# Performance work log

Hardware: AMD Instinct MI355X
Metric: run time of the kernel (lower is better)

Reference implementation:

```python
import jax, jax.numpy as jnp
import numpy as np

N_NODES = 10000
EPS = 1e-5


def _layernorm(x, gamma, beta):
    mu = jnp.mean(x, axis=-1, keepdims=True)
    var = jnp.mean(jnp.square(x - mu), axis=-1, keepdims=True)
    return (x - mu) * jax.lax.rsqrt(var + EPS) * gamma + beta


def _sage_pool_layer(h, src, dst, Wp, bp, Ws, Wn, b, gamma, beta):
    # DGL SAGEConv(aggregator='pool'):
    #   m_u = relu(h_u @ Wp^T + bp); h_neigh[v] = max_{u in N(v)} m_u (0 if no neighbors)
    #   rst = h @ Ws^T + h_neigh @ Wn^T + b
    m = jax.nn.relu(h @ Wp.T + bp)              # [N, d]
    msg = m[src]                                 # [E, d] gather
    agg = jax.ops.segment_max(msg, dst, num_segments=N_NODES)
    agg = jnp.where(jnp.isfinite(agg), agg, 0.0)  # isolated nodes -> 0
    rst = h @ Ws.T + agg @ Wn.T + b
    # gsage_layer: LayerNorm, then Encoder applies relu (dropout inactive in eval)
    return jax.nn.relu(_layernorm(rst, gamma, beta))


def setup_inputs() -> dict:
    key = jax.random.key(0)
    ks = jax.random.split(key, 16)
    d = 256
    E = 320000
    s = 1.0 / np.sqrt(d)
    inp = {
        "h": jax.random.normal(ks[0], (N_NODES, d), dtype=jnp.float32),
        "edge_src": jax.random.randint(ks[1], (E,), 0, N_NODES, dtype=jnp.int32),
        "edge_dst": jax.random.randint(ks[2], (E,), 0, N_NODES, dtype=jnp.int32),
    }
    for li in range(2):
        kk = jax.random.split(ks[3 + li], 3)
        inp[f"Wp{li}"] = jax.random.normal(kk[0], (d, d), dtype=jnp.float32) * s
        inp[f"bp{li}"] = jnp.zeros((d,), jnp.float32)
        inp[f"Ws{li}"] = jax.random.normal(kk[1], (d, d), dtype=jnp.float32) * s
        inp[f"Wn{li}"] = jax.random.normal(kk[2], (d, d), dtype=jnp.float32) * s
        inp[f"b{li}"] = jnp.zeros((d,), jnp.float32)
        inp[f"g{li}"] = jnp.ones((d,), jnp.float32)
        inp[f"be{li}"] = jnp.zeros((d,), jnp.float32)
    return inp


def reference(h, edge_src, edge_dst,
              Wp0, bp0, Ws0, Wn0, b0, g0, be0,
              Wp1, bp1, Ws1, Wn1, b1, g1, be1):
    h = _sage_pool_layer(h, edge_src, edge_dst, Wp0, bp0, Ws0, Wn0, b0, g0, be0)
    h = _sage_pool_layer(h, edge_src, edge_dst, Wp1, bp1, Ws1, Wn1, b1, g1, be1)
    return h
```

## Files before the change

kernel.cpp:

```cpp
#include <hip/hip_runtime.h>

#define D 256
#define CAP 128
#define ASTRIDE 280
#define LN_EPS 1e-5f

typedef short short8 __attribute__((ext_vector_type(8)));
typedef float floatx4 __attribute__((ext_vector_type(4)));
typedef unsigned short u16x4 __attribute__((ext_vector_type(4)));

typedef const __attribute__((address_space(1))) void* gas_t;
typedef __attribute__((address_space(3))) void* las_t;

#define WAIT_VM(n) __builtin_amdgcn_s_waitcnt(((n) & 0xF) | (((n) >> 4) << 14) | (7 << 4) | (0xF << 8))

__device__ __forceinline__ u16x4 umax4(u16x4 a, u16x4 b) {
#if __has_builtin(__builtin_elementwise_max)
    return __builtin_elementwise_max(a, b);
#else
    u16x4 r;
    r.x = a.x > b.x ? a.x : b.x; r.y = a.y > b.y ? a.y : b.y;
    r.z = a.z > b.z ? a.z : b.z; r.w = a.w > b.w ? a.w : b.w;
    return r;
#endif
}

__device__ __forceinline__ unsigned short f2b(float f) {
    union { float f; unsigned int u; } x; x.f = f;
    unsigned int u = x.u + 0x7FFFu + ((x.u >> 16) & 1u);
    return (unsigned short)(u >> 16);
}

__global__ __launch_bounds__(256) void prep_kernel(
    const float* __restrict__ w0, const float* __restrict__ w1,
    const float* __restrict__ w2, const float* __restrict__ w3,
    const float* __restrict__ w4, const float* __restrict__ w5,
    unsigned short* __restrict__ wb,
    const float* __restrict__ h, unsigned short* __restrict__ hb, int nh4,
    int* __restrict__ cnt, unsigned short* __restrict__ mb, int N)
{
    const int blk = blockIdx.x;
    const int tid = threadIdx.x;
    if (blk < 384) {
        const int wsel = blk >> 6;
        const float* src;
        switch (wsel) {
            case 0: src = w0; break; case 1: src = w1; break;
            case 2: src = w2; break; case 3: src = w3; break;
            case 4: src = w4; break; default: src = w5; break;
        }
        const int idx = (blk & 63) * 1024 + tid * 4;
        const float4 v = *(const float4*)(src + idx);
        ushort4 o;
        o.x = f2b(v.x); o.y = f2b(v.y); o.z = f2b(v.z); o.w = f2b(v.w);
        *(ushort4*)(wb + (size_t)wsel * 65536 + idx) = o;
    } else if (blk < 1024) {
        int i = (blk - 384) * 256 + tid;
        const int stride = 640 * 256;
        for (; i < nh4; i += stride) {
            const float4 v = *(const float4*)(h + (size_t)i * 4);
            ushort4 o;
            o.x = f2b(v.x); o.y = f2b(v.y); o.z = f2b(v.z); o.w = f2b(v.w);
            *(ushort4*)(hb + (size_t)i * 4) = o;
        }
    } else if (blk < 1064) {
        const int i = (blk - 1024) * 256 + tid;
        if (i < N) cnt[i] = 0;
    } else {
        mb[(size_t)N * D + tid] = 0;
    }
}

__global__ __launch_bounds__(256) void gemm_relu(
    const unsigned short* __restrict__ A, const unsigned short* __restrict__ W,
    const float* __restrict__ bias, unsigned short* __restrict__ out_b, int N,
    const int* __restrict__ esrc, const int* __restrict__ edst,
    int* __restrict__ cnt, unsigned short* __restrict__ csr, int E, int ngemm)
{
    if ((int)blockIdx.x >= ngemm) {
        const int nsb = gridDim.x - ngemm;
        int i = ((int)blockIdx.x - ngemm) * 256 + threadIdx.x;
        const int stride = nsb * 256;
        for (; i < E; i += stride) {
            const int d = edst[i];
            const int pos = atomicAdd(&cnt[d], 1);
            if (pos < CAP) csr[(size_t)d * CAP + pos] = (unsigned short)esrc[i];
        }
        return;
    }

    const int tid = threadIdx.x;
    const int wave = tid >> 6;
    const int lane = tid & 63;
    const int quad = lane >> 4;
    const int l16 = lane & 15;
    const int row0 = blockIdx.x * 16;
    const int koff = quad * 8;

    floatx4 acc[4];
#pragma unroll
    for (int t = 0; t < 4; t++) acc[t] = (floatx4)(0.f);

    const unsigned short* aptr = A + (size_t)(row0 + l16) * D + koff;
    const unsigned short* wptr = W + (size_t)(wave * 64 + l16) * D + koff;
#pragma unroll
    for (int k0 = 0; k0 < D; k0 += 32) {
        const short8 av = *(const short8*)(aptr + k0);
        const short8 b0 = *(const short8*)(wptr + k0);
        const short8 b1 = *(const short8*)(wptr + 16 * D + k0);
        const short8 b2 = *(const short8*)(wptr + 32 * D + k0);
        const short8 b3 = *(const short8*)(wptr + 48 * D + k0);
        acc[0] = __builtin_amdgcn_mfma_f32_16x16x32_bf16(av, b0, acc[0], 0, 0, 0);
        acc[1] = __builtin_amdgcn_mfma_f32_16x16x32_bf16(av, b1, acc[1], 0, 0, 0);
        acc[2] = __builtin_amdgcn_mfma_f32_16x16x32_bf16(av, b2, acc[2], 0, 0, 0);
        acc[3] = __builtin_amdgcn_mfma_f32_16x16x32_bf16(av, b3, acc[3], 0, 0, 0);
    }

#pragma unroll
    for (int t = 0; t < 4; t++) {
        const float bcol = bias[wave * 64 + t * 16 + l16];
#pragma unroll
        for (int r = 0; r < 4; r++) {
            const int rg = row0 + quad * 4 + r;
            const int col = wave * 64 + t * 16 + l16;
            out_b[(size_t)rg * D + col] = f2b(fmaxf(acc[t][r] + bcol, 0.f));
        }
    }
}

__global__ __launch_bounds__(256, 3) void gemm_ln_pool(
    const unsigned short* __restrict__ A, const unsigned short* __restrict__ Wself,
    const unsigned short* __restrict__ Wneigh,
    const unsigned short* __restrict__ mpool,
    const int* __restrict__ cnt, const unsigned short* __restrict__ csr,
    const float* __restrict__ bias,
    const float* __restrict__ gamma, const float* __restrict__ beta,
    unsigned short* __restrict__ out_b, float* __restrict__ out_f, int N)
{
    __shared__ unsigned short idxS[16][CAP];
    __shared__ unsigned short gbuf[4][2][8][D];
    __shared__ unsigned short aggS[16 * ASTRIDE];
    __shared__ float redS[4][16], redS2[4][16], muA[16], rsA[16];

    const int tid = threadIdx.x;
    const int wave = tid >> 6;
    const int lane = tid & 63;
    const int quad = lane >> 4;
    const int l16 = lane & 15;
    const int row0 = blockIdx.x * 16;
    const int koff = quad * 8;
    const int rbase = wave * 4;
    const int half = lane >> 5;
    const int l32 = lane & 31;

    int degs[4];
#pragma unroll
    for (int rr = 0; rr < 4; rr++) degs[rr] = min(cnt[row0 + rbase + rr], CAP);
    int P = max(max(degs[0], degs[1]), max(degs[2], degs[3]));
    const int P2 = (P + 1) & ~1;
#pragma unroll
    for (int rr = 0; rr < 4; rr++) {
        const int rg = row0 + rbase + rr;
        for (int i = lane; i < P2; i += 64)
            idxS[rbase + rr][i] = (i < degs[rr]) ? csr[(size_t)rg * CAP + i]
                                                 : (unsigned short)N;
    }

    floatx4 acc[4];
#pragma unroll
    for (int t = 0; t < 4; t++) acc[t] = (floatx4)(0.f);

    {
        const unsigned short* aptr = A + (size_t)(row0 + l16) * D + koff;
        const unsigned short* wptr = Wself + (size_t)(wave * 64 + l16) * D + koff;
#pragma unroll
        for (int k0 = 0; k0 < D; k0 += 32) {
            const short8 av = *(const short8*)(aptr + k0);
            const short8 b0 = *(const short8*)(wptr + k0);
            const short8 b1 = *(const short8*)(wptr + 16 * D + k0);
            const short8 b2 = *(const short8*)(wptr + 32 * D + k0);
            const short8 b3 = *(const short8*)(wptr + 48 * D + k0);
            acc[0] = __builtin_amdgcn_mfma_f32_16x16x32_bf16(av, b0, acc[0], 0, 0, 0);
            acc[1] = __builtin_amdgcn_mfma_f32_16x16x32_bf16(av, b1, acc[1], 0, 0, 0);
            acc[2] = __builtin_amdgcn_mfma_f32_16x16x32_bf16(av, b2, acc[2], 0, 0, 0);
            acc[3] = __builtin_amdgcn_mfma_f32_16x16x32_bf16(av, b3, acc[3], 0, 0, 0);
        }
    }

    {
        const int nb = P2 >> 1;
        u16x4 mx[4];
#pragma unroll
        for (int rr = 0; rr < 4; rr++) mx[rr] = (u16x4)(0);

#define ISSUE_BURST(bi, buf)                                                    \
        {                                                                       \
            _Pragma("unroll") for (int rr = 0; rr < 4; rr++) {                  \
                const int jj = idxS[rbase + rr][2 * (bi) + half];               \
                const unsigned short* g = mpool + (size_t)jj * D + l32 * 8;     \
                __builtin_amdgcn_global_load_lds(                               \
                    (gas_t)g, (las_t)&gbuf[wave][buf][rr * 2][0], 16, 0, 0);    \
            }                                                                   \
        }

        if (nb > 0) ISSUE_BURST(0, 0);
        if (nb > 1) ISSUE_BURST(1, 1);
        for (int b = 0; b < nb; b++) {
            if (b + 1 < nb) WAIT_VM(4); else WAIT_VM(0);
            const int buf = b & 1;
#pragma unroll
            for (int rr = 0; rr < 4; rr++) {
                const u16x4 a0 = *(const u16x4*)&gbuf[wave][buf][rr * 2 + 0][lane * 4];
                const u16x4 a1 = *(const u16x4*)&gbuf[wave][buf][rr * 2 + 1][lane * 4];
                mx[rr] = umax4(mx[rr], umax4(a0, a1));
            }
            if (b + 2 < nb) ISSUE_BURST(b + 2, buf);
        }
#undef ISSUE_BURST
#pragma unroll
        for (int rr = 0; rr < 4; rr++)
            *(u16x4*)&aggS[(rbase + rr) * ASTRIDE + lane * 4] = mx[rr];
    }
    __syncthreads();

    {
        const unsigned short* wptr = Wneigh + (size_t)(wave * 64 + l16) * D + koff;
#pragma unroll
        for (int k0 = 0; k0 < D; k0 += 32) {
            const short8 av = *(const short8*)&aggS[l16 * ASTRIDE + koff + k0];
            const short8 b0 = *(const short8*)(wptr + k0);
            const short8 b1 = *(const short8*)(wptr + 16 * D + k0);
            const short8 b2 = *(const short8*)(wptr + 32 * D + k0);
            const short8 b3 = *(const short8*)(wptr + 48 * D + k0);
            acc[0] = __builtin_amdgcn_mfma_f32_16x16x32_bf16(av, b0, acc[0], 0, 0, 0);
            acc[1] = __builtin_amdgcn_mfma_f32_16x16x32_bf16(av, b1, acc[1], 0, 0, 0);
            acc[2] = __builtin_amdgcn_mfma_f32_16x16x32_bf16(av, b2, acc[2], 0, 0, 0);
            acc[3] = __builtin_amdgcn_mfma_f32_16x16x32_bf16(av, b3, acc[3], 0, 0, 0);
        }
    }

    float bcol[4];
#pragma unroll
    for (int t = 0; t < 4; t++) bcol[t] = bias[wave * 64 + t * 16 + l16];
#pragma unroll
    for (int t = 0; t < 4; t++)
#pragma unroll
        for (int r = 0; r < 4; r++) acc[t][r] += bcol[t];

#pragma unroll
    for (int r = 0; r < 4; r++) {
        float s = 0.f, s2 = 0.f;
#pragma unroll
        for (int t = 0; t < 4; t++) {
            const float v = acc[t][r];
            s += v; s2 += v * v;
        }
        s += __shfl_xor(s, 1);  s2 += __shfl_xor(s2, 1);
        s += __shfl_xor(s, 2);  s2 += __shfl_xor(s2, 2);
        s += __shfl_xor(s, 4);  s2 += __shfl_xor(s2, 4);
        s += __shfl_xor(s, 8);  s2 += __shfl_xor(s2, 8);
        if (l16 == 0) {
            redS[wave][quad * 4 + r] = s;
            redS2[wave][quad * 4 + r] = s2;
        }
    }
    __syncthreads();
    if (tid < 16) {
        const float S  = redS[0][tid] + redS[1][tid] + redS[2][tid] + redS[3][tid];
        const float S2 = redS2[0][tid] + redS2[1][tid] + redS2[2][tid] + redS2[3][tid];
        const float mu = S * (1.f / D);
        float var = S2 * (1.f / D) - mu * mu;
        var = fmaxf(var, 0.f);
        muA[tid] = mu;
        rsA[tid] = rsqrtf(var + LN_EPS);
    }
    __syncthreads();

    float gcol[4], becol[4];
#pragma unroll
    for (int t = 0; t < 4; t++) {
        gcol[t] = gamma[wave * 64 + t * 16 + l16];
        becol[t] = beta[wave * 64 + t * 16 + l16];
    }
#pragma unroll
    for (int r = 0; r < 4; r++) {
        const int rl = quad * 4 + r;
        const int rg = row0 + rl;
        const float mu = muA[rl];
        const float rs = rsA[rl];
#pragma unroll
        for (int t = 0; t < 4; t++) {
            const int col = wave * 64 + t * 16 + l16;
            float o = (acc[t][r] - mu) * rs * gcol[t] + becol[t];
            o = fmaxf(o, 0.f);
            if (out_f) out_f[(size_t)rg * D + col] = o;
            else       out_b[(size_t)rg * D + col] = f2b(o);
        }
    }
}

extern "C" void kernel_launch(void* const* d_in, const int* in_sizes, int n_in,
                              void* d_out, int out_size, void* d_ws, size_t ws_size,
                              hipStream_t stream) {
    const float* h    = (const float*)d_in[0];
    const int*   esrc = (const int*)d_in[1];
    const int*   edst = (const int*)d_in[2];
    const float* Wp0  = (const float*)d_in[3];
    const float* bp0  = (const float*)d_in[4];
    const float* Ws0  = (const float*)d_in[5];
    const float* Wn0  = (const float*)d_in[6];
    const float* b0   = (const float*)d_in[7];
    const float* g0   = (const float*)d_in[8];
    const float* be0  = (const float*)d_in[9];
    const float* Wp1  = (const float*)d_in[10];
    const float* bp1  = (const float*)d_in[11];
    const float* Ws1  = (const float*)d_in[12];
    const float* Wn1  = (const float*)d_in[13];
    const float* b1   = (const float*)d_in[14];
    const float* g1   = (const float*)d_in[15];
    const float* be1  = (const float*)d_in[16];

    const int N = in_sizes[0] / D;
    const int E = in_sizes[1];
    const size_t ND = (size_t)N * D;

    unsigned short* hb  = (unsigned short*)d_ws;
    unsigned short* mb  = hb + ND;
    unsigned short* h1b = mb + ND + D;
    unsigned short* wb  = h1b + ND;
    int* cnt = (int*)(wb + 6 * 65536);
    unsigned short* csr = (unsigned short*)(cnt + N);

    unsigned short* wpb0 = wb + 0 * 65536;
    unsigned short* wsb0 = wb + 1 * 65536;
    unsigned short* wnb0 = wb + 2 * 65536;
    unsigned short* wpb1 = wb + 3 * 65536;
    unsigned short* wsb1 = wb + 4 * 65536;
    unsigned short* wnb1 = wb + 5 * 65536;

    const int gblocks = N / 16;
    const int sblocks = 128;

    prep_kernel<<<1065, 256, 0, stream>>>(Wp0, Ws0, Wn0, Wp1, Ws1, Wn1, wb,
                                          h, hb, (int)(ND / 4), cnt, mb, N);

    gemm_relu<<<gblocks + sblocks, 256, 0, stream>>>(hb, wpb0, bp0, mb, N,
                                                     esrc, edst, cnt, csr, E, gblocks);
    gemm_ln_pool<<<gblocks, 256, 0, stream>>>(hb, wsb0, wnb0, mb, cnt, csr,
                                              b0, g0, be0, h1b, nullptr, N);

    gemm_relu<<<gblocks, 256, 0, stream>>>(h1b, wpb1, bp1, mb, N,
                                           esrc, edst, cnt, csr, 0, gblocks);
    gemm_ln_pool<<<gblocks, 256, 0, stream>>>(h1b, wsb1, wnb1, mb, cnt, csr,
                                              b1, g1, be1, nullptr, (float*)d_out, N);
}
```

Measured before the change: 222.2 us.

## Batch GEMM fragment loads and deepen neighbor-gather bursts to four rows

Restructures the MFMA loops so that all A and B fragments for half of K are loaded up front, giving more loads in flight before the MFMAs run. Each neighbor max-pool burst now gathers four neighbor rows per target node instead of two, with a doubled LDS gather buffer and a higher vmcnt wait threshold. Launch-bound occupancy hints change, and more scatter blocks are used for CSR construction. The trade-off is higher register and LDS use, which lowers occupancy in the pool kernel, and extra padding work for low-degree nodes.

```diff
diff --git a/kernel.cpp b/kernel.cpp
--- a/kernel.cpp
+++ b/kernel.cpp
@@ -30,6 +30,22 @@
     unsigned int u = x.u + 0x7FFFu + ((x.u >> 16) & 1u);
     return (unsigned short)(u >> 16);
 }
+
+#define GEMM_HALF(APTR_EXPR, WPTR, K0H)                                         \
+    {                                                                           \
+        short8 aF[4], bF[4][4];                                                 \
+        _Pragma("unroll") for (int ks = 0; ks < 4; ks++)                        \
+            aF[ks] = APTR_EXPR(K0H + ks * 32);                                  \
+        _Pragma("unroll") for (int ks = 0; ks < 4; ks++)                        \
+        _Pragma("unroll") for (int t = 0; t < 4; t++)                           \
+            bF[ks][t] = *(const short8*)((WPTR) + t * 16 * D + (K0H) + ks * 32);\
+        _Pragma("unroll") for (int ks = 0; ks < 4; ks++) {                      \
+            acc[0] = __builtin_amdgcn_mfma_f32_16x16x32_bf16(aF[ks], bF[ks][0], acc[0], 0, 0, 0); \
+            acc[1] = __builtin_amdgcn_mfma_f32_16x16x32_bf16(aF[ks], bF[ks][1], acc[1], 0, 0, 0); \
+            acc[2] = __builtin_amdgcn_mfma_f32_16x16x32_bf16(aF[ks], bF[ks][2], acc[2], 0, 0, 0); \
+            acc[3] = __builtin_amdgcn_mfma_f32_16x16x32_bf16(aF[ks], bF[ks][3], acc[3], 0, 0, 0); \
+        }                                                                       \
+    }
 
 __global__ __launch_bounds__(256) void prep_kernel(
     const float* __restrict__ w0, const float* __restrict__ w1,
@@ -71,7 +87,7 @@
     }
 }
 
-__global__ __launch_bounds__(256) void gemm_relu(
+__global__ __launch_bounds__(256, 4) void gemm_relu(
     const unsigned short* __restrict__ A, const unsigned short* __restrict__ W,
     const float* __restrict__ bias, unsigned short* __restrict__ out_b, int N,
     const int* __restrict__ esrc, const int* __restrict__ edst,
@@ -103,18 +119,10 @@
 
     const unsigned short* aptr = A + (size_t)(row0 + l16) * D + koff;
     const unsigned short* wptr = W + (size_t)(wave * 64 + l16) * D + koff;
-#pragma unroll
-    for (int k0 = 0; k0 < D; k0 += 32) {
-        const short8 av = *(const short8*)(aptr + k0);
-        const short8 b0 = *(const short8*)(wptr + k0);
-        const short8 b1 = *(const short8*)(wptr + 16 * D + k0);
-        const short8 b2 = *(const short8*)(wptr + 32 * D + k0);
-        const short8 b3 = *(const short8*)(wptr + 48 * D + k0);
-        acc[0] = __builtin_amdgcn_mfma_f32_16x16x32_bf16(av, b0, acc[0], 0, 0, 0);
-        acc[1] = __builtin_amdgcn_mfma_f32_16x16x32_bf16(av, b1, acc[1], 0, 0, 0);
-        acc[2] = __builtin_amdgcn_mfma_f32_16x16x32_bf16(av, b2, acc[2], 0, 0, 0);
-        acc[3] = __builtin_amdgcn_mfma_f32_16x16x32_bf16(av, b3, acc[3], 0, 0, 0);
-    }
+#define A_GLOBAL(K) (*(const short8*)(aptr + (K)))
+    GEMM_HALF(A_GLOBAL, wptr, 0)
+    GEMM_HALF(A_GLOBAL, wptr, 128)
+#undef A_GLOBAL
 
 #pragma unroll
     for (int t = 0; t < 4; t++) {
@@ -128,7 +136,7 @@
     }
 }
 
-__global__ __launch_bounds__(256, 3) void gemm_ln_pool(
+__global__ __launch_bounds__(256, 2) void gemm_ln_pool(
     const unsigned short* __restrict__ A, const unsigned short* __restrict__ Wself,
     const unsigned short* __restrict__ Wneigh,
     const unsigned short* __restrict__ mpool,
@@ -138,7 +146,7 @@
     unsigned short* __restrict__ out_b, float* __restrict__ out_f, int N)
 {
     __shared__ unsigned short idxS[16][CAP];
-    __shared__ unsigned short gbuf[4][2][8][D];
+    __shared__ unsigned short gbuf[4][2][16][D];
     __shared__ unsigned short aggS[16 * ASTRIDE];
     __shared__ float redS[4][16], redS2[4][16], muA[16], rsA[16];
 
@@ -157,11 +165,11 @@
 #pragma unroll
     for (int rr = 0; rr < 4; rr++) degs[rr] = min(cnt[row0 + rbase + rr], CAP);
     int P = max(max(degs[0], degs[1]), max(degs[2], degs[3]));
-    const int P2 = (P + 1) & ~1;
+    const int P4 = (P + 3) & ~3;
 #pragma unroll
     for (int rr = 0; rr < 4; rr++) {
         const int rg = row0 + rbase + rr;
-        for (int i = lane; i < P2; i += 64)
+        for (int i = lane; i < P4; i += 64)
             idxS[rbase + rr][i] = (i < degs[rr]) ? csr[(size_t)rg * CAP + i]
                                                  : (unsigned short)N;
     }
@@ -173,22 +181,14 @@
     {
         const unsigned short* aptr = A + (size_t)(row0 + l16) * D + koff;
         const unsigned short* wptr = Wself + (size_t)(wave * 64 + l16) * D + koff;
-#pragma unroll
-        for (int k0 = 0; k0 < D; k0 += 32) {
-            const short8 av = *(const short8*)(aptr + k0);
-            const short8 b0 = *(const short8*)(wptr + k0);
-            const short8 b1 = *(const short8*)(wptr + 16 * D + k0);
-            const short8 b2 = *(const short8*)(wptr + 32 * D + k0);
-            const short8 b3 = *(const short8*)(wptr + 48 * D + k0);
-            acc[0] = __builtin_amdgcn_mfma_f32_16x16x32_bf16(av, b0, acc[0], 0, 0, 0);
-            acc[1] = __builtin_amdgcn_mfma_f32_16x16x32_bf16(av, b1, acc[1], 0, 0, 0);
-            acc[2] = __builtin_amdgcn_mfma_f32_16x16x32_bf16(av, b2, acc[2], 0, 0, 0);
-            acc[3] = __builtin_amdgcn_mfma_f32_16x16x32_bf16(av, b3, acc[3], 0, 0, 0);
-        }
+#define A_GLOBAL(K) (*(const short8*)(aptr + (K)))
+        GEMM_HALF(A_GLOBAL, wptr, 0)
+        GEMM_HALF(A_GLOBAL, wptr, 128)
+#undef A_GLOBAL
     }
 
     {
-        const int nb = P2 >> 1;
+        const int nb = P4 >> 2;
         u16x4 mx[4];
 #pragma unroll
         for (int rr = 0; rr < 4; rr++) mx[rr] = (u16x4)(0);
@@ -196,23 +196,29 @@
 #define ISSUE_BURST(bi, buf)                                                    \
         {                                                                       \
             _Pragma("unroll") for (int rr = 0; rr < 4; rr++) {                  \
-                const int jj = idxS[rbase + rr][2 * (bi) + half];               \
-                const unsigned short* g = mpool + (size_t)jj * D + l32 * 8;     \
+                const int j0 = idxS[rbase + rr][4 * (bi) + half];               \
+                const int j1 = idxS[rbase + rr][4 * (bi) + 2 + half];           \
+                const unsigned short* g0 = mpool + (size_t)j0 * D + l32 * 8;    \
+                const unsigned short* g1 = mpool + (size_t)j1 * D + l32 * 8;    \
                 __builtin_amdgcn_global_load_lds(                               \
-                    (gas_t)g, (las_t)&gbuf[wave][buf][rr * 2][0], 16, 0, 0);    \
+                    (gas_t)g0, (las_t)&gbuf[wave][buf][rr * 4][0], 16, 0, 0);   \
+                __builtin_amdgcn_global_load_lds(                               \
+                    (gas_t)g1, (las_t)&gbuf[wave][buf][rr * 4 + 2][0], 16, 0, 0); \
             }                                                                   \
         }
 
         if (nb > 0) ISSUE_BURST(0, 0);
         if (nb > 1) ISSUE_BURST(1, 1);
         for (int b = 0; b < nb; b++) {
-            if (b + 1 < nb) WAIT_VM(4); else WAIT_VM(0);
+            if (b + 1 < nb) WAIT_VM(8); else WAIT_VM(0);
             const int buf = b & 1;
 #pragma unroll
             for (int rr = 0; rr < 4; rr++) {
-                const u16x4 a0 = *(const u16x4*)&gbuf[wave][buf][rr * 2 + 0][lane * 4];
-                const u16x4 a1 = *(const u16x4*)&gbuf[wave][buf][rr * 2 + 1][lane * 4];
-                mx[rr] = umax4(mx[rr], umax4(a0, a1));
+                const u16x4 a0 = *(const u16x4*)&gbuf[wave][buf][rr * 4 + 0][lane * 4];
+                const u16x4 a1 = *(const u16x4*)&gbuf[wave][buf][rr * 4 + 1][lane * 4];
+                const u16x4 a2 = *(const u16x4*)&gbuf[wave][buf][rr * 4 + 2][lane * 4];
+                const u16x4 a3 = *(const u16x4*)&gbuf[wave][buf][rr * 4 + 3][lane * 4];
+                mx[rr] = umax4(mx[rr], umax4(umax4(a0, a1), umax4(a2, a3)));
             }
             if (b + 2 < nb) ISSUE_BURST(b + 2, buf);
         }
@@ -225,18 +231,10 @@
 
     {
         const unsigned short* wptr = Wneigh + (size_t)(wave * 64 + l16) * D + koff;
-#pragma unroll
-        for (int k0 = 0; k0 < D; k0 += 32) {
-            const short8 av = *(const short8*)&aggS[l16 * ASTRIDE + koff + k0];
-            const short8 b0 = *(const short8*)(wptr + k0);
-            const short8 b1 = *(const short8*)(wptr + 16 * D + k0);
-            const short8 b2 = *(const short8*)(wptr + 32 * D + k0);
-            const short8 b3 = *(const short8*)(wptr + 48 * D + k0);
-            acc[0] = __builtin_amdgcn_mfma_f32_16x16x32_bf16(av, b0, acc[0], 0, 0, 0);
-            acc[1] = __builtin_amdgcn_mfma_f32_16x16x32_bf16(av, b1, acc[1], 0, 0, 0);
-            acc[2] = __builtin_amdgcn_mfma_f32_16x16x32_bf16(av, b2, acc[2], 0, 0, 0);
-            acc[3] = __builtin_amdgcn_mfma_f32_16x16x32_bf16(av, b3, acc[3], 0, 0, 0);
-        }
+#define A_LDS(K) (*(const short8*)&aggS[l16 * ASTRIDE + koff + (K)])
+        GEMM_HALF(A_LDS, wptr, 0)
+        GEMM_HALF(A_LDS, wptr, 128)
+#undef A_LDS
     }
 
     float bcol[4];
@@ -339,7 +337,7 @@
     unsigned short* wnb1 = wb + 5 * 65536;
 
     const int gblocks = N / 16;
-    const int sblocks = 128;
+    const int sblocks = 192;
 
     prep_kernel<<<1065, 256, 0, stream>>>(Wp0, Ws0, Wn0, Wp1, Ws1, Wn1, wb,
                                           h, hb, (int)(ND / 4), cnt, mb, N);
```

After: 233.6 us. 1.05x slower.

## Split gemm_relu into single-wave blocks with batched MFMA operand loads

Applied to the files above, without the earlier changes.

The pool-projection GEMM now launches one 64-thread wave per 16x64 output tile, four times as many blocks as before, and gives each block its own column offset instead of four waves sharing a row tile. The K loop is restructured into two halves. Each half preloads four A fragments and sixteen B fragments before issuing its MFMAs, to expose more memory-level parallelism. The edge-scatter part of the fused kernel also gets more, smaller blocks (1024 blocks of 64 threads). This trades a higher block count and more registers per wave for better latency hiding and finer load balancing.

```diff
diff --git a/kernel.cpp b/kernel.cpp
--- a/kernel.cpp
+++ b/kernel.cpp
@@ -30,6 +30,22 @@
     unsigned int u = x.u + 0x7FFFu + ((x.u >> 16) & 1u);
     return (unsigned short)(u >> 16);
 }
+
+#define GEMM_HALF(APTR_EXPR, WPTR, K0H)                                         \
+    {                                                                           \
+        short8 aF[4], bF[4][4];                                                 \
+        _Pragma("unroll") for (int ks = 0; ks < 4; ks++)                        \
+            aF[ks] = APTR_EXPR(K0H + ks * 32);                                  \
+        _Pragma("unroll") for (int ks = 0; ks < 4; ks++)                        \
+        _Pragma("unroll") for (int t = 0; t < 4; t++)                           \
+            bF[ks][t] = *(const short8*)((WPTR) + t * 16 * D + (K0H) + ks * 32);\
+        _Pragma("unroll") for (int ks = 0; ks < 4; ks++) {                      \
+            acc[0] = __builtin_amdgcn_mfma_f32_16x16x32_bf16(aF[ks], bF[ks][0], acc[0], 0, 0, 0); \
+            acc[1] = __builtin_amdgcn_mfma_f32_16x16x32_bf16(aF[ks], bF[ks][1], acc[1], 0, 0, 0); \
+            acc[2] = __builtin_amdgcn_mfma_f32_16x16x32_bf16(aF[ks], bF[ks][2], acc[2], 0, 0, 0); \
+            acc[3] = __builtin_amdgcn_mfma_f32_16x16x32_bf16(aF[ks], bF[ks][3], acc[3], 0, 0, 0); \
+        }                                                                       \
+    }
 
 __global__ __launch_bounds__(256) void prep_kernel(
     const float* __restrict__ w0, const float* __restrict__ w1,
@@ -71,7 +87,7 @@
     }
 }
 
-__global__ __launch_bounds__(256) void gemm_relu(
+__global__ __launch_bounds__(64, 4) void gemm_relu(
     const unsigned short* __restrict__ A, const unsigned short* __restrict__ W,
     const float* __restrict__ bias, unsigned short* __restrict__ out_b, int N,
     const int* __restrict__ esrc, const int* __restrict__ edst,
@@ -79,8 +95,8 @@
 {
     if ((int)blockIdx.x >= ngemm) {
         const int nsb = gridDim.x - ngemm;
-        int i = ((int)blockIdx.x - ngemm) * 256 + threadIdx.x;
-        const int stride = nsb * 256;
+        int i = ((int)blockIdx.x - ngemm) * 64 + threadIdx.x;
+        const int stride = nsb * 64;
         for (; i < E; i += stride) {
             const int d = edst[i];
             const int pos = atomicAdd(&cnt[d], 1);
@@ -89,12 +105,12 @@
         return;
     }
 
-    const int tid = threadIdx.x;
-    const int wave = tid >> 6;
-    const int lane = tid & 63;
+    const int lane = threadIdx.x;
     const int quad = lane >> 4;
     const int l16 = lane & 15;
-    const int row0 = blockIdx.x * 16;
+    const int blk = blockIdx.x;
+    const int row0 = (blk >> 2) * 16;
+    const int col0 = (blk & 3) * 64;
     const int koff = quad * 8;
 
     floatx4 acc[4];
@@ -102,27 +118,19 @@
     for (int t = 0; t < 4; t++) acc[t] = (floatx4)(0.f);
 
     const unsigned short* aptr = A + (size_t)(row0 + l16) * D + koff;
-    const unsigned short* wptr = W + (size_t)(wave * 64 + l16) * D + koff;
-#pragma unroll
-    for (int k0 = 0; k0 < D; k0 += 32) {
-        const short8 av = *(const short8*)(aptr + k0);
-        const short8 b0 = *(const short8*)(wptr + k0);
-        const short8 b1 = *(const short8*)(wptr + 16 * D + k0);
-        const short8 b2 = *(const short8*)(wptr + 32 * D + k0);
-        const short8 b3 = *(const short8*)(wptr + 48 * D + k0);
-        acc[0] = __builtin_amdgcn_mfma_f32_16x16x32_bf16(av, b0, acc[0], 0, 0, 0);
-        acc[1] = __builtin_amdgcn_mfma_f32_16x16x32_bf16(av, b1, acc[1], 0, 0, 0);
-        acc[2] = __builtin_amdgcn_mfma_f32_16x16x32_bf16(av, b2, acc[2], 0, 0, 0);
-        acc[3] = __builtin_amdgcn_mfma_f32_16x16x32_bf16(av, b3, acc[3], 0, 0, 0);
-    }
+    const unsigned short* wptr = W + (size_t)(col0 + l16) * D + koff;
+#define A_GLOBAL(K) (*(const short8*)(aptr + (K)))
+    GEMM_HALF(A_GLOBAL, wptr, 0)
+    GEMM_HALF(A_GLOBAL, wptr, 128)
+#undef A_GLOBAL
 
 #pragma unroll
     for (int t = 0; t < 4; t++) {
-        const float bcol = bias[wave * 64 + t * 16 + l16];
+        const float bcol = bias[col0 + t * 16 + l16];
 #pragma unroll
         for (int r = 0; r < 4; r++) {
             const int rg = row0 + quad * 4 + r;
-            const int col = wave * 64 + t * 16 + l16;
+            const int col = col0 + t * 16 + l16;
             out_b[(size_t)rg * D + col] = f2b(fmaxf(acc[t][r] + bcol, 0.f));
         }
     }
@@ -338,19 +346,20 @@
     unsigned short* wsb1 = wb + 4 * 65536;
     unsigned short* wnb1 = wb + 5 * 65536;
 
-    const int gblocks = N / 16;
-    const int sblocks = 128;
+    const int rblocks = (N / 16) * 4;
+    const int pblocks = N / 16;
+    const int sblocks = 1024;
 
     prep_kernel<<<1065, 256, 0, stream>>>(Wp0, Ws0, Wn0, Wp1, Ws1, Wn1, wb,
                                           h, hb, (int)(ND / 4), cnt, mb, N);
 
-    gemm_relu<<<gblocks + sblocks, 256, 0, stream>>>(hb, wpb0, bp0, mb, N,
-                                                     esrc, edst, cnt, csr, E, gblocks);
-    gemm_ln_pool<<<gblocks, 256, 0, stream>>>(hb, wsb0, wnb0, mb, cnt, csr,
+    gemm_relu<<<rblocks + sblocks, 64, 0, stream>>>(hb, wpb0, bp0, mb, N,
+                                                    esrc, edst, cnt, csr, E, rblocks);
+    gemm_ln_pool<<<pblocks, 256, 0, stream>>>(hb, wsb0, wnb0, mb, cnt, csr,
                                               b0, g0, be0, h1b, nullptr, N);
 
-    gemm_relu<<<gblocks, 256, 0, stream>>>(h1b, wpb1, bp1, mb, N,
-                                           esrc, edst, cnt, csr, 0, gblocks);
-    gemm_ln_pool<<<gblocks, 256, 0, stream>>>(h1b, wsb1, wnb1, mb, cnt, csr,
+    gemm_relu<<<rblocks, 64, 0, stream>>>(h1b, wpb1, bp1, mb, N,
+                                          esrc, edst, cnt, csr, 0, rblocks);
+    gemm_ln_pool<<<pblocks, 256, 0, stream>>>(h1b, wsb1, wnb1, mb, cnt, csr,
                                               b1, g1, be1, nullptr, (float*)d_out, N);
 }
```

Measured after the change: 216.1 us. -2.7%, faster.
